# Performance work log

Measured on AMD Instinct MI355X. Metric: run time of the kernel, lower is better.

## Reference

```python
import jax, jax.numpy as jnp
import numpy as np

B, DIN, G, W, D, L = 65536, 256, 4, 128, 4, 3  # batch, in_feat, groups, group width, list_depth, group_depth
H = G * W  # 512 hidden width


def setup_inputs() -> dict:
    key = jax.random.key(0)
    k0, k1, k2 = jax.random.split(key, 3)
    x = jax.random.normal(k0, (B, DIN), dtype=jnp.float32)
    W0 = jax.random.normal(k1, (DIN, H), dtype=jnp.float32) * 0.05
    b0 = jnp.zeros((H,), dtype=jnp.float32)
    Wg = jax.random.normal(k2, (L, G, D, W, W), dtype=jnp.float32) * 0.05
    bg = jnp.zeros((L, G, D, W), dtype=jnp.float32)
    return {"x": x, "W0": W0, "b0": b0, "Wg": Wg, "bg": bg}


def reference(x, W0, b0, Wg, bg):
    # initial Dense(H, relu)
    x0 = jax.nn.relu(x @ W0 + b0)  # [B, H]
    b = x0.shape[0]
    # split into G contiguous groups of width W (== tf.split axis=1)
    h = x0.reshape(b, G, W)  # [B, G, W]
    for l in range(L):  # group_depth stacked GroupDenseHybrid layers
        resid = h
        for d in range(D):  # ListDenseHybrid: chain of Dense(W, relu), batched over groups
            h = jax.nn.relu(jnp.einsum('bgk,gkn->bgn', h, Wg[l, :, d]) + bg[l, :, d][None, :, :])
        # skip_fn='relu' applied to (branch_out + group_input); concat == reshape back
        h = jax.nn.relu(h + resid)
    out = jax.nn.relu(h.reshape(b, H) + x0)  # final residual + relu (no norm layer)
    return out
```

## Files before the change

### kernel.cpp

```cpp
#include <hip/hip_runtime.h>
#include <stdint.h>

typedef __bf16 bf16_t;
typedef __bf16 bf16x8 __attribute__((ext_vector_type(8)));
typedef __bf16 bf16x4 __attribute__((ext_vector_type(4)));
typedef float  f32x16 __attribute__((ext_vector_type(16)));
typedef float  f32x4  __attribute__((ext_vector_type(4)));

#define MFMA_B16(a, b, c) __builtin_amdgcn_mfma_f32_32x32x16_bf16((a), (b), (c), 0, 0, 0)

static constexpr int kG = 4, kD = 4, kH = 512;
static constexpr int kW0T = 4 * 256 * 128;
static constexpr int kWgT = 3 * 4 * 4 * 128 * 128;

__device__ __host__ inline int sigma_tile(int n) {
  int gi = n >> 3, h = (n >> 2) & 1, r = n & 3;
  return 16 * (gi & 1) + 8 * h + 4 * (gi >> 1) + r;
}

__global__ __launch_bounds__(256) void prep_weights(
    const float* __restrict__ W0, const float* __restrict__ Wg,
    bf16_t* __restrict__ w0t, bf16_t* __restrict__ wgt)
{
  int e = blockIdx.x * 256 + threadIdx.x;
  if (e < kW0T) {
    int g  = e >> 15;
    int r  = e & 32767;
    int f  = r >> 9;
    int ln = (r >> 3) & 63;
    int j  = r & 7;
    int kt = f >> 2, nt = f & 3;
    int col = nt * 32 + sigma_tile(ln & 31);
    int k   = kt * 16 + ((ln >> 5) << 3) + j;
    w0t[e] = (bf16_t)W0[k * kH + g * 128 + col];
  } else if (e < kW0T + kWgT) {
    int e2 = e - kW0T;
    int g  = e2 / (12 * 16384);
    int r2 = e2 - g * (12 * 16384);
    int m  = r2 >> 14;
    int r  = r2 & 16383;
    int f  = r >> 9;
    int ln = (r >> 3) & 63;
    int j  = r & 7;
    int kt = f >> 2, nt = f & 3;
    int col = nt * 32 + sigma_tile(ln & 31);
    int k   = kt * 16 + ((ln >> 5) << 3) + j;
    int l   = m >> 2, d = m & 3;
    wgt[e2] = (bf16_t)Wg[((((l * kG + g) * kD + d) * 128) + k) * 128 + col];
  }
}

__global__ __launch_bounds__(256, 2) void resnext_fused(
    const float* __restrict__ x, const float* __restrict__ b0,
    const float* __restrict__ bg, const bf16_t* __restrict__ w0t,
    const bf16_t* __restrict__ wgt, float* __restrict__ out)
{
  __shared__ bf16_t sW[2][16384];
  __shared__ float  sBias[13 * 128];

  const int tid = threadIdx.x;
  const int ln  = tid & 63;
  const int wv  = tid >> 6;
  const int l31 = ln & 31;
  const int l5  = ln >> 5;

  const int g  = blockIdx.x >> 9;
  const int r0 = (blockIdx.x & 511) << 7;

  const bf16_t* wgt_g = wgt + g * (12 * 16384);

  for (int i = tid; i < 13 * 128; i += 256) {
    float v;
    if (i < 128) v = b0[g * 128 + i];
    else {
      int m = (i - 128) >> 7, u = (i - 128) & 127;
      int l = m >> 2, d = m & 3;
      v = bg[((l * kG + g) * kD + d) * 128 + u];
    }
    sBias[i] = v;
  }

  auto stage = [&](int m, int buf) {
    #pragma unroll
    for (int i = 0; i < 8; ++i) {
      int frag = wv * 8 + i;
      __builtin_amdgcn_global_load_lds(
          (const __attribute__((address_space(1))) void*)(wgt_g + m * 16384 + frag * 512 + ln * 8),
          (__attribute__((address_space(3))) void*)(&sW[buf][frag * 512]),
          16, 0, 0);
    }
  };

  stage(0, 0);

  f32x16 acc[4];
  #pragma unroll
  for (int t = 0; t < 4; ++t)
    #pragma unroll
    for (int q = 0; q < 16; ++q) acc[t][q] = 0.f;

  {
    const bf16_t* w0g = w0t + g * 32768;
    const float* xb = x + (size_t)(r0 + wv * 32 + l31) * 256 + l5 * 8;
    #pragma unroll
    for (int kt = 0; kt < 16; ++kt) {
      f32x4 xa = *(const f32x4*)(xb + kt * 16);
      f32x4 xc = *(const f32x4*)(xb + kt * 16 + 4);
      bf16x8 bfr;
      #pragma unroll
      for (int q = 0; q < 4; ++q) {
        bfr[q]     = (bf16_t)xa[q];
        bfr[q + 4] = (bf16_t)xc[q];
      }
      #pragma unroll
      for (int nt = 0; nt < 4; ++nt) {
        bf16x8 a = *(const bf16x8*)(w0g + (kt * 4 + nt) * 512 + ln * 8);
        acc[nt] = MFMA_B16(a, bfr, acc[nt]);
      }
    }
  }
  __syncthreads();

  bf16x8 keepA[4], keepB[4], x0A[4], x0B[4], resA[4], resB[4];

  #pragma unroll
  for (int t = 0; t < 4; ++t) {
    #pragma unroll
    for (int gi = 0; gi < 4; ++gi) {
      f32x4 bv = *(const f32x4*)(sBias + 32 * t + 16 * (gi & 1) + 8 * l5 + 4 * (gi >> 1));
      #pragma unroll
      for (int r = 0; r < 4; ++r) {
        float v = acc[t][gi * 4 + r] + bv[r];
        v = fmaxf(v, 0.f);
        bf16_t o = (bf16_t)v;
        int half = (gi >> 1) * 4 + r;
        if (gi & 1) keepB[t][half] = o; else keepA[t][half] = o;
      }
    }
    x0A[t] = keepA[t]; x0B[t] = keepB[t];
    resA[t] = keepA[t]; resB[t] = keepB[t];
  }

  #pragma unroll 1
  for (int m = 0; m < 12; ++m) {
    if (m < 11) stage(m + 1, (m + 1) & 1);

    const bf16_t* wb = sW[m & 1];
    #pragma unroll
    for (int t = 0; t < 4; ++t)
      #pragma unroll
      for (int q = 0; q < 16; ++q) acc[t][q] = 0.f;

    #pragma unroll
    for (int kt = 0; kt < 8; ++kt) {
      bf16x8 bfr = (kt & 1) ? keepB[kt >> 1] : keepA[kt >> 1];
      #pragma unroll
      for (int nt = 0; nt < 4; ++nt) {
        bf16x8 a = *(const bf16x8*)(wb + (kt * 4 + nt) * 512 + ln * 8);
        acc[nt] = MFMA_B16(a, bfr, acc[nt]);
      }
    }

    const bool layer_end = ((m & 3) == 3);
    const float* bptr = sBias + (m + 1) * 128;

    if (m < 11) {
      #pragma unroll
      for (int t = 0; t < 4; ++t) {
        #pragma unroll
        for (int gi = 0; gi < 4; ++gi) {
          f32x4 bv = *(const f32x4*)(bptr + 32 * t + 16 * (gi & 1) + 8 * l5 + 4 * (gi >> 1));
          #pragma unroll
          for (int r = 0; r < 4; ++r) {
            float v = acc[t][gi * 4 + r] + bv[r];
            v = fmaxf(v, 0.f);
            if (layer_end) {
              bf16x8 src = (gi & 1) ? resB[t] : resA[t];
              v += (float)src[(gi >> 1) * 4 + r];
              v = fmaxf(v, 0.f);
            }
            bf16_t o = (bf16_t)v;
            int half = (gi >> 1) * 4 + r;
            if (gi & 1) keepB[t][half] = o; else keepA[t][half] = o;
          }
        }
        if (layer_end) { resA[t] = keepA[t]; resB[t] = keepB[t]; }
      }
      __syncthreads();
    } else {
      float fin[4][16];
      #pragma unroll
      for (int t = 0; t < 4; ++t) {
        #pragma unroll
        for (int gi = 0; gi < 4; ++gi) {
          f32x4 bv = *(const f32x4*)(bptr + 32 * t + 16 * (gi & 1) + 8 * l5 + 4 * (gi >> 1));
          #pragma unroll
          for (int r = 0; r < 4; ++r) {
            float v = acc[t][gi * 4 + r] + bv[r];
            v = fmaxf(v, 0.f);
            bf16x8 rs = (gi & 1) ? resB[t] : resA[t];
            v += (float)rs[(gi >> 1) * 4 + r];
            v = fmaxf(v, 0.f);
            bf16x8 xs = (gi & 1) ? x0B[t] : x0A[t];
            v += (float)xs[(gi >> 1) * 4 + r];
            v = fmaxf(v, 0.f);
            fin[t][gi * 4 + r] = v;
          }
        }
      }
      __syncthreads();

      float* sT = (float*)sW;
      const int row = wv * 32 + l31;
      #pragma unroll
      for (int t = 0; t < 4; ++t) {
        #pragma unroll
        for (int gi = 0; gi < 4; ++gi) {
          int u = 32 * t + 16 * (gi & 1) + 8 * l5 + 4 * (gi >> 1);
          int col_s = u ^ ((l31 & 7) << 2);
          f32x4 v;
          #pragma unroll
          for (int r = 0; r < 4; ++r) v[r] = fin[t][gi * 4 + r];
          *(f32x4*)(sT + row * 128 + col_s) = v;
        }
      }
      __syncthreads();

      #pragma unroll
      for (int it = 0; it < 16; ++it) {
        int chunk = it * 256 + tid;
        int rw = chunk >> 5, c = chunk & 31;
        int col_s = (4 * c) ^ ((rw & 7) << 2);
        f32x4 v = *(const f32x4*)(sT + rw * 128 + col_s);
        *(f32x4*)(out + (size_t)(r0 + rw) * kH + g * 128 + 4 * c) = v;
      }
    }
  }
}

extern "C" void kernel_launch(void* const* d_in, const int* in_sizes, int n_in,
                              void* d_out, int out_size, void* d_ws, size_t ws_size,
                              hipStream_t stream) {
  const float* x  = (const float*)d_in[0];
  const float* W0 = (const float*)d_in[1];
  const float* b0 = (const float*)d_in[2];
  const float* Wg = (const float*)d_in[3];
  const float* bg = (const float*)d_in[4];
  float* outp = (float*)d_out;

  bf16_t* w0t = (bf16_t*)d_ws;
  bf16_t* wgt = w0t + kW0T;

  const int prep_total = kW0T + kWgT;
  prep_weights<<<(prep_total + 255) / 256, 256, 0, stream>>>(W0, Wg, w0t, wgt);

  resnext_fused<<<2048, 256, 0, stream>>>(x, b0, bg, w0t, wgt, outp);
}
```

Before: 458.8 us.

## Stream weight fragments from global memory into registers instead of LDS staging

Removes the double-buffered LDS staging of per-layer weights via global_load_lds and instead loads each weight fragment straight from global (L2-cached) memory into registers, with a one-k-step software prefetch into alternating register sets. This drops the per-layer __syncthreads barriers and cuts LDS use to the output transpose buffer. The trade-off is more vector registers and global/L2 loads issued by every wave instead of shared LDS reads, with latency hidden only one k-step ahead. Occupancy and register pressure may change.

```diff
diff --git a/kernel.cpp b/kernel.cpp
--- a/kernel.cpp
+++ b/kernel.cpp
@@ -55,8 +55,8 @@
     const float* __restrict__ bg, const bf16_t* __restrict__ w0t,
     const bf16_t* __restrict__ wgt, float* __restrict__ out)
 {
-  __shared__ bf16_t sW[2][16384];
-  __shared__ float  sBias[13 * 128];
+  __shared__ float sT[128 * 128];
+  __shared__ float sBias[13 * 128];
 
   const int tid = threadIdx.x;
   const int ln  = tid & 63;
@@ -80,19 +80,6 @@
     sBias[i] = v;
   }
 
-  auto stage = [&](int m, int buf) {
-    #pragma unroll
-    for (int i = 0; i < 8; ++i) {
-      int frag = wv * 8 + i;
-      __builtin_amdgcn_global_load_lds(
-          (const __attribute__((address_space(1))) void*)(wgt_g + m * 16384 + frag * 512 + ln * 8),
-          (__attribute__((address_space(3))) void*)(&sW[buf][frag * 512]),
-          16, 0, 0);
-    }
-  };
-
-  stage(0, 0);
-
   f32x16 acc[4];
   #pragma unroll
   for (int t = 0; t < 4; ++t)
@@ -119,6 +106,14 @@
       }
     }
   }
+
+  bf16x8 a0[4], a1[4];
+  {
+    const bf16_t* wl0 = wgt_g + ln * 8;
+    #pragma unroll
+    for (int nt = 0; nt < 4; ++nt) a0[nt] = *(const bf16x8*)(wl0 + nt * 512);
+  }
+
   __syncthreads();
 
   bf16x8 keepA[4], keepB[4], x0A[4], x0B[4], resA[4], resB[4];
@@ -143,9 +138,9 @@
 
   #pragma unroll 1
   for (int m = 0; m < 12; ++m) {
-    if (m < 11) stage(m + 1, (m + 1) & 1);
-
-    const bf16_t* wb = sW[m & 1];
+    const bf16_t* wl  = wgt_g + m * 16384 + ln * 8;
+    const bf16_t* wlN = wl + 16384;
+
     #pragma unroll
     for (int t = 0; t < 4; ++t)
       #pragma unroll
@@ -153,12 +148,21 @@
 
     #pragma unroll
     for (int kt = 0; kt < 8; ++kt) {
+      if (kt < 7) {
+        #pragma unroll
+        for (int nt = 0; nt < 4; ++nt) {
+          bf16x8 v = *(const bf16x8*)(wl + ((kt + 1) * 4 + nt) * 512);
+          if (kt & 1) a0[nt] = v; else a1[nt] = v;
+        }
+      } else if (m < 11) {
+        #pragma unroll
+        for (int nt = 0; nt < 4; ++nt)
+          a0[nt] = *(const bf16x8*)(wlN + nt * 512);
+      }
       bf16x8 bfr = (kt & 1) ? keepB[kt >> 1] : keepA[kt >> 1];
       #pragma unroll
-      for (int nt = 0; nt < 4; ++nt) {
-        bf16x8 a = *(const bf16x8*)(wb + (kt * 4 + nt) * 512 + ln * 8);
-        acc[nt] = MFMA_B16(a, bfr, acc[nt]);
-      }
+      for (int nt = 0; nt < 4; ++nt)
+        acc[nt] = MFMA_B16((kt & 1) ? a1[nt] : a0[nt], bfr, acc[nt]);
     }
 
     const bool layer_end = ((m & 3) == 3);
@@ -186,7 +190,6 @@
         }
         if (layer_end) { resA[t] = keepA[t]; resB[t] = keepB[t]; }
       }
-      __syncthreads();
     } else {
       float fin[4][16];
       #pragma unroll
@@ -208,9 +211,7 @@
           }
         }
       }
-      __syncthreads();
-
-      float* sT = (float*)sW;
+
       const int row = wv * 32 + l31;
       #pragma unroll
       for (int t = 0; t < 4; ++t) {
```

After: 531.1 us. +15.7%, slower.

## Switch to 16x16x32 MFMA, 64-row tiles, single LDS buffer, 4 blocks/CU

Applied to the files above, without the earlier changes.

Replaces the 32x32x16 bf16 MFMA with the 16x16x32 variant and re-permutes the prepacked weight fragments to match. Each block now handles 64 rows instead of 128, and the grid doubles to 4096 blocks with an interleaved block-to-(group,row) mapping. Weight staging moves from double-buffered to a single LDS buffer, with the next stage issued after compute behind a raw barrier. Launch bounds rise to 4 blocks per CU so that occupancy, rather than intra-block double buffering, hides load latency. The cost is less overlap within a block and twice as many weight reloads per row tile.

```diff
diff --git a/kernel.cpp b/kernel.cpp
--- a/kernel.cpp
+++ b/kernel.cpp
@@ -3,19 +3,16 @@
 
 typedef __bf16 bf16_t;
 typedef __bf16 bf16x8 __attribute__((ext_vector_type(8)));
-typedef __bf16 bf16x4 __attribute__((ext_vector_type(4)));
-typedef float  f32x16 __attribute__((ext_vector_type(16)));
 typedef float  f32x4  __attribute__((ext_vector_type(4)));
 
-#define MFMA_B16(a, b, c) __builtin_amdgcn_mfma_f32_32x32x16_bf16((a), (b), (c), 0, 0, 0)
+#define MFMA16(a, b, c) __builtin_amdgcn_mfma_f32_16x16x32_bf16((a), (b), (c), 0, 0, 0)
 
 static constexpr int kG = 4, kD = 4, kH = 512;
 static constexpr int kW0T = 4 * 256 * 128;
 static constexpr int kWgT = 3 * 4 * 4 * 128 * 128;
 
-__device__ __host__ inline int sigma_tile(int n) {
-  int gi = n >> 3, h = (n >> 2) & 1, r = n & 3;
-  return 16 * (gi & 1) + 8 * h + 4 * (gi >> 1) + r;
+__device__ __host__ inline int sigma16(int p) {
+  return (p & 3) + 4 * ((p >> 4) & 1) + 8 * ((p >> 2) & 3) + 32 * (p >> 5);
 }
 
 __global__ __launch_bounds__(256) void prep_weights(
@@ -29,9 +26,9 @@
     int f  = r >> 9;
     int ln = (r >> 3) & 63;
     int j  = r & 7;
-    int kt = f >> 2, nt = f & 3;
-    int col = nt * 32 + sigma_tile(ln & 31);
-    int k   = kt * 16 + ((ln >> 5) << 3) + j;
+    int ktl = f >> 3, nt = f & 7;
+    int col = sigma16(nt * 16 + (ln & 15));
+    int k   = ktl * 32 + ((ln >> 4) << 3) + j;
     w0t[e] = (bf16_t)W0[k * kH + g * 128 + col];
   } else if (e < kW0T + kWgT) {
     int e2 = e - kW0T;
@@ -42,30 +39,32 @@
     int f  = r >> 9;
     int ln = (r >> 3) & 63;
     int j  = r & 7;
-    int kt = f >> 2, nt = f & 3;
-    int col = nt * 32 + sigma_tile(ln & 31);
-    int k   = kt * 16 + ((ln >> 5) << 3) + j;
+    int ktl = f >> 3, nt = f & 7;
+    int col = sigma16(nt * 16 + (ln & 15));
+    int k   = ktl * 32 + ((ln >> 4) << 3) + j;
     int l   = m >> 2, d = m & 3;
     wgt[e2] = (bf16_t)Wg[((((l * kG + g) * kD + d) * 128) + k) * 128 + col];
   }
 }
 
-__global__ __launch_bounds__(256, 2) void resnext_fused(
+__global__ __launch_bounds__(256, 4) void resnext_fused(
     const float* __restrict__ x, const float* __restrict__ b0,
     const float* __restrict__ bg, const bf16_t* __restrict__ w0t,
     const bf16_t* __restrict__ wgt, float* __restrict__ out)
 {
-  __shared__ bf16_t sW[2][16384];
+  __shared__ bf16_t sW[16384];
   __shared__ float  sBias[13 * 128];
 
   const int tid = threadIdx.x;
   const int ln  = tid & 63;
   const int wv  = tid >> 6;
-  const int l31 = ln & 31;
-  const int l5  = ln >> 5;
-
-  const int g  = blockIdx.x >> 9;
-  const int r0 = (blockIdx.x & 511) << 7;
+  const int l15 = ln & 15;
+  const int c4  = ln >> 4;
+
+  const int bid     = blockIdx.x;
+  const int logical = (bid & 7) * 512 + (bid >> 3);
+  const int g  = logical & 3;
+  const int r0 = (logical >> 2) << 6;
 
   const bf16_t* wgt_g = wgt + g * (12 * 16384);
 
@@ -80,32 +79,32 @@
     sBias[i] = v;
   }
 
-  auto stage = [&](int m, int buf) {
+  auto stage = [&](int m) {
     #pragma unroll
     for (int i = 0; i < 8; ++i) {
       int frag = wv * 8 + i;
       __builtin_amdgcn_global_load_lds(
           (const __attribute__((address_space(1))) void*)(wgt_g + m * 16384 + frag * 512 + ln * 8),
-          (__attribute__((address_space(3))) void*)(&sW[buf][frag * 512]),
+          (__attribute__((address_space(3))) void*)(&sW[frag * 512]),
           16, 0, 0);
     }
   };
 
-  stage(0, 0);
-
-  f32x16 acc[4];
+  stage(0);
+
+  f32x4 acc[8];
   #pragma unroll
-  for (int t = 0; t < 4; ++t)
-    #pragma unroll
-    for (int q = 0; q < 16; ++q) acc[t][q] = 0.f;
+  for (int nt = 0; nt < 8; ++nt)
+    #pragma unroll
+    for (int q = 0; q < 4; ++q) acc[nt][q] = 0.f;
 
   {
     const bf16_t* w0g = w0t + g * 32768;
-    const float* xb = x + (size_t)(r0 + wv * 32 + l31) * 256 + l5 * 8;
-    #pragma unroll
-    for (int kt = 0; kt < 16; ++kt) {
-      f32x4 xa = *(const f32x4*)(xb + kt * 16);
-      f32x4 xc = *(const f32x4*)(xb + kt * 16 + 4);
+    const float* xb = x + (size_t)(r0 + wv * 16 + l15) * 256 + c4 * 8;
+    #pragma unroll
+    for (int ktl = 0; ktl < 8; ++ktl) {
+      f32x4 xa = *(const f32x4*)(xb + ktl * 32);
+      f32x4 xc = *(const f32x4*)(xb + ktl * 32 + 4);
       bf16x8 bfr;
       #pragma unroll
       for (int q = 0; q < 4; ++q) {
@@ -113,121 +112,100 @@
         bfr[q + 4] = (bf16_t)xc[q];
       }
       #pragma unroll
-      for (int nt = 0; nt < 4; ++nt) {
-        bf16x8 a = *(const bf16x8*)(w0g + (kt * 4 + nt) * 512 + ln * 8);
-        acc[nt] = MFMA_B16(a, bfr, acc[nt]);
+      for (int nt = 0; nt < 8; ++nt) {
+        bf16x8 a = *(const bf16x8*)(w0g + (ktl * 8 + nt) * 512 + ln * 8);
+        acc[nt] = MFMA16(a, bfr, acc[nt]);
       }
     }
   }
   __syncthreads();
 
-  bf16x8 keepA[4], keepB[4], x0A[4], x0B[4], resA[4], resB[4];
+  bf16x8 keep[4], x0v[4], resv[4];
 
   #pragma unroll
-  for (int t = 0; t < 4; ++t) {
-    #pragma unroll
-    for (int gi = 0; gi < 4; ++gi) {
-      f32x4 bv = *(const f32x4*)(sBias + 32 * t + 16 * (gi & 1) + 8 * l5 + 4 * (gi >> 1));
-      #pragma unroll
-      for (int r = 0; r < 4; ++r) {
-        float v = acc[t][gi * 4 + r] + bv[r];
-        v = fmaxf(v, 0.f);
-        bf16_t o = (bf16_t)v;
-        int half = (gi >> 1) * 4 + r;
-        if (gi & 1) keepB[t][half] = o; else keepA[t][half] = o;
-      }
-    }
-    x0A[t] = keepA[t]; x0B[t] = keepB[t];
-    resA[t] = keepA[t]; resB[t] = keepB[t];
-  }
+  for (int nt = 0; nt < 8; ++nt) {
+    const int ub = 4 * (nt & 1) + 8 * c4 + 32 * (nt >> 1);
+    f32x4 bv = *(const f32x4*)(sBias + ub);
+    #pragma unroll
+    for (int q = 0; q < 4; ++q) {
+      float v = fmaxf(acc[nt][q] + bv[q], 0.f);
+      keep[nt >> 1][4 * (nt & 1) + q] = (bf16_t)v;
+    }
+  }
+  #pragma unroll
+  for (int t = 0; t < 4; ++t) { x0v[t] = keep[t]; resv[t] = keep[t]; }
 
   #pragma unroll 1
   for (int m = 0; m < 12; ++m) {
-    if (m < 11) stage(m + 1, (m + 1) & 1);
-
-    const bf16_t* wb = sW[m & 1];
-    #pragma unroll
-    for (int t = 0; t < 4; ++t)
-      #pragma unroll
-      for (int q = 0; q < 16; ++q) acc[t][q] = 0.f;
-
-    #pragma unroll
-    for (int kt = 0; kt < 8; ++kt) {
-      bf16x8 bfr = (kt & 1) ? keepB[kt >> 1] : keepA[kt >> 1];
-      #pragma unroll
-      for (int nt = 0; nt < 4; ++nt) {
-        bf16x8 a = *(const bf16x8*)(wb + (kt * 4 + nt) * 512 + ln * 8);
-        acc[nt] = MFMA_B16(a, bfr, acc[nt]);
-      }
-    }
+    #pragma unroll
+    for (int nt = 0; nt < 8; ++nt)
+      #pragma unroll
+      for (int q = 0; q < 4; ++q) acc[nt][q] = 0.f;
+
+    #pragma unroll
+    for (int ktl = 0; ktl < 4; ++ktl) {
+      bf16x8 bfr = keep[ktl];
+      #pragma unroll
+      for (int nt = 0; nt < 8; ++nt) {
+        bf16x8 a = *(const bf16x8*)(sW + (ktl * 8 + nt) * 512 + ln * 8);
+        acc[nt] = MFMA16(a, bfr, acc[nt]);
+      }
+    }
+
+    asm volatile("s_waitcnt lgkmcnt(0)\n\ts_barrier" ::: "memory");
+    if (m < 11) stage(m + 1);
 
     const bool layer_end = ((m & 3) == 3);
     const float* bptr = sBias + (m + 1) * 128;
 
     if (m < 11) {
       #pragma unroll
-      for (int t = 0; t < 4; ++t) {
-        #pragma unroll
-        for (int gi = 0; gi < 4; ++gi) {
-          f32x4 bv = *(const f32x4*)(bptr + 32 * t + 16 * (gi & 1) + 8 * l5 + 4 * (gi >> 1));
-          #pragma unroll
-          for (int r = 0; r < 4; ++r) {
-            float v = acc[t][gi * 4 + r] + bv[r];
-            v = fmaxf(v, 0.f);
-            if (layer_end) {
-              bf16x8 src = (gi & 1) ? resB[t] : resA[t];
-              v += (float)src[(gi >> 1) * 4 + r];
-              v = fmaxf(v, 0.f);
-            }
-            bf16_t o = (bf16_t)v;
-            int half = (gi >> 1) * 4 + r;
-            if (gi & 1) keepB[t][half] = o; else keepA[t][half] = o;
-          }
+      for (int nt = 0; nt < 8; ++nt) {
+        const int ub = 4 * (nt & 1) + 8 * c4 + 32 * (nt >> 1);
+        f32x4 bv = *(const f32x4*)(bptr + ub);
+        #pragma unroll
+        for (int q = 0; q < 4; ++q) {
+          float v = fmaxf(acc[nt][q] + bv[q], 0.f);
+          if (layer_end)
+            v = fmaxf(v + (float)resv[nt >> 1][4 * (nt & 1) + q], 0.f);
+          keep[nt >> 1][4 * (nt & 1) + q] = (bf16_t)v;
         }
-        if (layer_end) { resA[t] = keepA[t]; resB[t] = keepB[t]; }
+      }
+      if (layer_end) {
+        #pragma unroll
+        for (int t = 0; t < 4; ++t) resv[t] = keep[t];
+      }
+      asm volatile("s_waitcnt vmcnt(0)\n\ts_barrier" ::: "memory");
+    } else {
+      float fin[8][4];
+      #pragma unroll
+      for (int nt = 0; nt < 8; ++nt) {
+        const int ub = 4 * (nt & 1) + 8 * c4 + 32 * (nt >> 1);
+        f32x4 bv = *(const f32x4*)(bptr + ub);
+        #pragma unroll
+        for (int q = 0; q < 4; ++q) {
+          float v = fmaxf(acc[nt][q] + bv[q], 0.f);
+          v = fmaxf(v + (float)resv[nt >> 1][4 * (nt & 1) + q], 0.f);
+          v = fmaxf(v + (float)x0v[nt >> 1][4 * (nt & 1) + q], 0.f);
+          fin[nt][q] = v;
+        }
+      }
+
+      float* sT = (float*)sW;
+      const int row = wv * 16 + l15;
+      #pragma unroll
+      for (int nt = 0; nt < 8; ++nt) {
+        const int ub = 4 * (nt & 1) + 8 * c4 + 32 * (nt >> 1);
+        int col_s = ub ^ ((l15 & 7) << 2);
+        f32x4 v;
+        #pragma unroll
+        for (int q = 0; q < 4; ++q) v[q] = fin[nt][q];
+        *(f32x4*)(sT + row * 128 + col_s) = v;
       }
       __syncthreads();
-    } else {
-      float fin[4][16];
-      #pragma unroll
-      for (int t = 0; t < 4; ++t) {
-        #pragma unroll
-        for (int gi = 0; gi < 4; ++gi) {
-          f32x4 bv = *(const f32x4*)(bptr + 32 * t + 16 * (gi & 1) + 8 * l5 + 4 * (gi >> 1));
-          #pragma unroll
-          for (int r = 0; r < 4; ++r) {
-            float v = acc[t][gi * 4 + r] + bv[r];
-            v = fmaxf(v, 0.f);
-            bf16x8 rs = (gi & 1) ? resB[t] : resA[t];
-            v += (float)rs[(gi >> 1) * 4 + r];
-            v = fmaxf(v, 0.f);
-            bf16x8 xs = (gi & 1) ? x0B[t] : x0A[t];
-            v += (float)xs[(gi >> 1) * 4 + r];
-            v = fmaxf(v, 0.f);
-            fin[t][gi * 4 + r] = v;
-          }
-        }
-      }
-      __syncthreads();
-
-      float* sT = (float*)sW;
-      const int row = wv * 32 + l31;
-      #pragma unroll
-      for (int t = 0; t < 4; ++t) {
-        #pragma unroll
-        for (int gi = 0; gi < 4; ++gi) {
-          int u = 32 * t + 16 * (gi & 1) + 8 * l5 + 4 * (gi >> 1);
-          int col_s = u ^ ((l31 & 7) << 2);
-          f32x4 v;
-          #pragma unroll
-          for (int r = 0; r < 4; ++r) v[r] = fin[t][gi * 4 + r];
-          *(f32x4*)(sT + row * 128 + col_s) = v;
-        }
-      }
-      __syncthreads();
-
-      #pragma unroll
-      for (int it = 0; it < 16; ++it) {
+
+      #pragma unroll
+      for (int it = 0; it < 8; ++it) {
         int chunk = it * 256 + tid;
         int rw = chunk >> 5, c = chunk & 31;
         int col_s = (4 * c) ^ ((rw & 7) << 2);
@@ -254,5 +232,5 @@
   const int prep_total = kW0T + kWgT;
   prep_weights<<<(prep_total + 255) / 256, 256, 0, stream>>>(W0, Wg, w0t, wgt);
 
-  resnext_fused<<<2048, 256, 0, stream>>>(x, b0, bg, w0t, wgt, outp);
-}
+  resnext_fused<<<4096, 256, 0, stream>>>(x, b0, bg, w0t, wgt, outp);
+}
```

Measured after the change: 404.8 us. 11.8% less time.
